# Kernel tuning notes

Measured on AMD Instinct MI355X. Metric: run time of the kernel, lower is better.

Reference implementation:

```python
import jax, jax.numpy as jnp
import numpy as np

N = 50000
F_IN = 128
HID = 64
HEADS = 4
CLASSES = 16
E = 800000
NEG_SLOPE = 0.2


def _gat_layer(x, src, dst, W, a_src, a_dst, bias, heads, ch, concat):
    n = x.shape[0]
    h = (x @ W).reshape(n, heads, ch)                     # [N,H,C]
    alpha_src = jnp.einsum('nhc,hc->nh', h, a_src)        # [N,H]
    alpha_dst = jnp.einsum('nhc,hc->nh', h, a_dst)        # [N,H]
    e = jax.nn.leaky_relu(alpha_src[src] + alpha_dst[dst], NEG_SLOPE)  # [E,H]
    # segment softmax over edges grouped by destination node
    m = jax.ops.segment_max(e, dst, num_segments=n)       # [N,H]
    ex = jnp.exp(e - m[dst])                              # [E,H]
    s = jax.ops.segment_sum(ex, dst, num_segments=n)      # [N,H]
    alpha = ex / (s[dst] + 1e-16)                         # [E,H]
    # weighted scatter-add aggregation of neighbor features
    out = jax.ops.segment_sum(h[src] * alpha[:, :, None], dst, num_segments=n)  # [N,H,C]
    if concat:
        return out.reshape(n, heads * ch) + bias
    return out.mean(axis=1) + bias


def setup_inputs() -> dict:
    key = jax.random.key(0)
    ks = jax.random.split(key, 12)
    x = jax.random.normal(ks[0], (N, F_IN), dtype=jnp.float32)
    edge_index = jax.random.randint(ks[1], (2, E), 0, N, dtype=jnp.int64)
    g1 = 1.0 / np.sqrt(F_IN)
    g2 = 1.0 / np.sqrt(HID * HEADS)
    W1 = jax.random.normal(ks[2], (F_IN, HEADS * HID), dtype=jnp.float32) * g1
    a_src1 = jax.random.normal(ks[3], (HEADS, HID), dtype=jnp.float32) * g1
    a_dst1 = jax.random.normal(ks[4], (HEADS, HID), dtype=jnp.float32) * g1
    b1 = jnp.zeros((HEADS * HID,), dtype=jnp.float32)
    W2 = jax.random.normal(ks[5], (HEADS * HID, CLASSES), dtype=jnp.float32) * g2
    a_src2 = jax.random.normal(ks[6], (1, CLASSES), dtype=jnp.float32) * g2
    a_dst2 = jax.random.normal(ks[7], (1, CLASSES), dtype=jnp.float32) * g2
    b2 = jnp.zeros((CLASSES,), dtype=jnp.float32)
    return {"x": x, "edge_index": edge_index, "W1": W1, "a_src1": a_src1,
            "a_dst1": a_dst1, "b1": b1, "W2": W2, "a_src2": a_src2,
            "a_dst2": a_dst2, "b2": b2}


def reference(x, edge_index, W1, a_src1, a_dst1, b1, W2, a_src2, a_dst2, b2):
    n = x.shape[0]
    # add self-loops (PyG GATConv default add_self_loops=True)
    loops = jnp.arange(n, dtype=edge_index.dtype)
    src = jnp.concatenate([edge_index[0], loops])
    dst = jnp.concatenate([edge_index[1], loops])
    h = _gat_layer(x, src, dst, W1, a_src1, a_dst1, b1, HEADS, HID, concat=True)
    h = jax.nn.elu(h)
    out = _gat_layer(h, src, dst, W2, a_src2, a_dst2, b2, 1, CLASSES, concat=False)
    return jax.nn.log_softmax(out, axis=1)
```

## Files before the change

kernel.cpp:

```cpp
#include <hip/hip_runtime.h>
#include <hip/hip_fp16.h>
#include <math.h>

#define NEG 0.2f

typedef __attribute__((ext_vector_type(8))) short bf16x8;
typedef __attribute__((ext_vector_type(4))) float f32x4;

__device__ __forceinline__ float lrelu(float x){ return x > 0.f ? x : NEG*x; }

__device__ __forceinline__ float bflo(unsigned u){ return __uint_as_float(u << 16); }
__device__ __forceinline__ float bfhi(unsigned u){ return __uint_as_float(u & 0xffff0000u); }

__device__ __forceinline__ float selh(float a0, float a1, float a2, float a3,
                                      bool bit0, bool bit1){
  float lo = bit0 ? a1 : a0;
  float hi = bit0 ? a3 : a2;
  return bit1 ? hi : lo;
}

__device__ __forceinline__ unsigned short f2bf(float x){
  unsigned u = __float_as_uint(x);
  u += 0x7fffu + ((u >> 16) & 1u);
  return (unsigned short)(u >> 16);
}

#define FMA8(e, h) \
  acc[0]=fmaf(e,bflo(h.x),acc[0]); acc[1]=fmaf(e,bfhi(h.x),acc[1]); \
  acc[2]=fmaf(e,bflo(h.y),acc[2]); acc[3]=fmaf(e,bfhi(h.y),acc[3]); \
  acc[4]=fmaf(e,bflo(h.z),acc[4]); acc[5]=fmaf(e,bfhi(h.z),acc[5]); \
  acc[6]=fmaf(e,bflo(h.w),acc[6]); acc[7]=fmaf(e,bfhi(h.w),acc[7]);

__global__ void detect_kernel(const int* __restrict__ ei, int* __restrict__ flag){
  int lane = threadIdx.x;
  int v = ei[2*lane + 1];
  unsigned long long b = __ballot(v != 0);
  if (lane == 0) flag[0] = (b == 0ULL) ? 1 : 0;
}

__global__ void fill_kernel(const int* __restrict__ ei, const int* __restrict__ flag,
                            int* __restrict__ cnt, int* __restrict__ adj, int E){
  int is64 = flag[0];
  int stride = gridDim.x * blockDim.x;
  for (int i = blockIdx.x*blockDim.x + threadIdx.x; i < E; i += stride){
    int s = is64 ? ei[2*i]       : ei[i];
    int d = is64 ? ei[2*(E + i)] : ei[E + i];
    int pos = atomicAdd(&cnt[d], 1);
    if (pos < 64) adj[(d << 6) + pos] = s;
  }
}

__device__ __forceinline__ int wt_addr(int col, int k){
  int g = (k >> 3) ^ (col & 7);
  return col*128 + g*8 + (k & 7);
}

__global__ __launch_bounds__(256) void gemm1_mfma(const float* __restrict__ x,
                             const float* __restrict__ W,
                             const float* __restrict__ asrcw, const float* __restrict__ adstw,
                             unsigned short* __restrict__ h1b,
                             float* __restrict__ as1, float* __restrict__ ad1, int N){
  __shared__ unsigned short wt[256*128];
  int t = threadIdx.x;
  int lane = t & 63, w = t >> 6;
  int row0 = blockIdx.x * 64 + w * 16;

  int arow = row0 + (lane & 15);
  if (arow >= N) arow = N - 1;
  const float* xr = x + (size_t)arow * 128 + (lane >> 4) * 8;
  bf16x8 afrag[4];
  #pragma unroll
  for (int kk = 0; kk < 4; kk++){
    float4 p0 = *reinterpret_cast<const float4*>(xr + kk*32);
    float4 p1 = *reinterpret_cast<const float4*>(xr + kk*32 + 4);
    afrag[kk][0] = (short)f2bf(p0.x); afrag[kk][1] = (short)f2bf(p0.y);
    afrag[kk][2] = (short)f2bf(p0.z); afrag[kk][3] = (short)f2bf(p0.w);
    afrag[kk][4] = (short)f2bf(p1.x); afrag[kk][5] = (short)f2bf(p1.y);
    afrag[kk][6] = (short)f2bf(p1.z); afrag[kk][7] = (short)f2bf(p1.w);
  }

  int c = t;
  for (int k0 = 0; k0 < 128; k0 += 8){
    bf16x8 v;
    #pragma unroll
    for (int j = 0; j < 8; j++) v[j] = (short)f2bf(W[(size_t)(k0+j)*256 + c]);
    *reinterpret_cast<bf16x8*>(&wt[wt_addr(c, k0)]) = v;
  }
  __syncthreads();

  f32x4 acc[16];
  #pragma unroll
  for (int n = 0; n < 16; n++) acc[n] = (f32x4){0.f,0.f,0.f,0.f};
  #pragma unroll
  for (int kk = 0; kk < 4; kk++){
    #pragma unroll
    for (int n = 0; n < 16; n++){
      bf16x8 b = *reinterpret_cast<const bf16x8*>(
          &wt[wt_addr(n*16 + (lane & 15), kk*32 + (lane >> 4)*8)]);
      acc[n] = __builtin_amdgcn_mfma_f32_16x16x32_bf16(afrag[kk], b, acc[n], 0, 0, 0);
    }
  }

  int rbase = row0 + (lane >> 4)*4;
  int cbase = lane & 15;
  #pragma unroll
  for (int n = 0; n < 16; n++){
    #pragma unroll
    for (int r = 0; r < 4; r++){
      int row = rbase + r;
      if (row < N) h1b[(size_t)row*256 + n*16 + cbase] = f2bf(acc[n][r]);
    }
  }

  float av[16], dv[16];
  #pragma unroll
  for (int n = 0; n < 16; n++){
    av[n] = asrcw[n*16 + cbase];
    dv[n] = adstw[n*16 + cbase];
  }
  #pragma unroll
  for (int r = 0; r < 4; r++){
    int row = rbase + r;
    float hs[4], hd[4];
    #pragma unroll
    for (int h = 0; h < 4; h++){
      float ps = 0.f, pd = 0.f;
      #pragma unroll
      for (int q = 0; q < 4; q++){
        int n = h*4 + q;
        ps = fmaf(acc[n][r], av[n], ps);
        pd = fmaf(acc[n][r], dv[n], pd);
      }
      #pragma unroll
      for (int off = 1; off < 16; off <<= 1){
        ps += __shfl_xor(ps, off, 64);
        pd += __shfl_xor(pd, off, 64);
      }
      hs[h] = ps; hd[h] = pd;
    }
    if (cbase == 0 && row < N){
      *reinterpret_cast<float4*>(as1 + (size_t)row*4) = make_float4(hs[0],hs[1],hs[2],hs[3]);
      *reinterpret_cast<float4*>(ad1 + (size_t)row*4) = make_float4(hd[0],hd[1],hd[2],hd[3]);
    }
  }
}

__global__ void edge_exp_kernel(const float* __restrict__ as1, const float* __restrict__ ad1,
                                const int* __restrict__ cnt, const int* __restrict__ adj,
                                __half* __restrict__ exarr, float* __restrict__ den, int N){
  int node = (blockIdx.x*blockDim.x + threadIdx.x) >> 6;
  int lane = threadIdx.x & 63;
  if (node >= N) return;
  int cn = cnt[node]; if (cn > 64) cn = 64;
  int beg = node << 6;
  bool val = lane < cn;
  int src = val ? adj[beg + lane] : 0;
  float4 dv = *reinterpret_cast<const float4*>(ad1 + (size_t)node*4);
  float4 sv = *reinterpret_cast<const float4*>(as1 + (size_t)src*4);
  float ex0 = val ? __expf(lrelu(sv.x + dv.x)) : 0.f;
  float ex1 = val ? __expf(lrelu(sv.y + dv.y)) : 0.f;
  float ex2 = val ? __expf(lrelu(sv.z + dv.z)) : 0.f;
  float ex3 = val ? __expf(lrelu(sv.w + dv.w)) : 0.f;

  if (val){
    __half2 p0 = __floats2half2_rn(ex0, ex1);
    __half2 p1 = __floats2half2_rn(ex2, ex3);
    uint2 o;
    o.x = *reinterpret_cast<unsigned*>(&p0);
    o.y = *reinterpret_cast<unsigned*>(&p1);
    *reinterpret_cast<uint2*>(exarr + (size_t)(beg + lane)*4) = o;
  }

  float sp0 = ex0, sp1 = ex1, sp2 = ex2, sp3 = ex3;
  #pragma unroll
  for (int off = 32; off; off >>= 1){
    sp0 += __shfl_xor(sp0, off, 64);
    sp1 += __shfl_xor(sp1, off, 64);
    sp2 += __shfl_xor(sp2, off, 64);
    sp3 += __shfl_xor(sp3, off, 64);
  }
  float4 s2 = *reinterpret_cast<const float4*>(as1 + (size_t)node*4);
  float exs0 = __expf(lrelu(s2.x + dv.x));
  float exs1 = __expf(lrelu(s2.y + dv.y));
  float exs2 = __expf(lrelu(s2.z + dv.z));
  float exs3 = __expf(lrelu(s2.w + dv.w));
  if (lane == 0){
    *reinterpret_cast<float4*>(den + (size_t)node*8) =
        make_float4(sp0 + exs0, sp1 + exs1, sp2 + exs2, sp3 + exs3);
    *reinterpret_cast<float4*>(den + (size_t)node*8 + 4) =
        make_float4(exs0, exs1, exs2, exs3);
  }
}

__global__ void agg1_kernel(const unsigned short* __restrict__ h1b,
                            const float* __restrict__ b1,
                            const int* __restrict__ cnt, const int* __restrict__ adj,
                            const __half* __restrict__ exarr, const float* __restrict__ den,
                            unsigned short* __restrict__ hact_b, int N){
  int node = (blockIdx.x*blockDim.x + threadIdx.x) >> 6;
  int lane = threadIdx.x & 63;
  if (node >= N) return;
  int cn = cnt[node]; if (cn > 64) cn = 64;
  int beg = node << 6;
  int hf = lane >> 5;
  int sl = lane & 31;
  int hh = sl >> 3;
  bool hb0 = (sl & 8) != 0, hb1 = (sl & 16) != 0;
  const __half* exw = exarr + (size_t)beg*4;
  const int* aj = adj + beg;
  unsigned co = sl*8;

  float acc[8];
  #pragma unroll
  for (int q = 0; q < 8; q++) acc[q] = 0.f;

  int j = 0;
  for (; j + 8 <= cn; j += 8){
    int e0 = j+hf, e1 = j+2+hf, e2 = j+4+hf, e3 = j+6+hf;
    int s0 = aj[e0], s1 = aj[e1], s2 = aj[e2], s3 = aj[e3];
    float w0 = __half2float(exw[e0*4+hh]);
    float w1 = __half2float(exw[e1*4+hh]);
    float w2 = __half2float(exw[e2*4+hh]);
    float w3 = __half2float(exw[e3*4+hh]);
    uint4 h0 = *reinterpret_cast<const uint4*>(h1b + (size_t)s0*256 + co);
    uint4 h1 = *reinterpret_cast<const uint4*>(h1b + (size_t)s1*256 + co);
    uint4 h2 = *reinterpret_cast<const uint4*>(h1b + (size_t)s2*256 + co);
    uint4 h3 = *reinterpret_cast<const uint4*>(h1b + (size_t)s3*256 + co);
    FMA8(w0, h0); FMA8(w1, h1); FMA8(w2, h2); FMA8(w3, h3);
  }
  for (; j + 4 <= cn; j += 4){
    int e0 = j+hf, e1 = j+2+hf;
    int s0 = aj[e0], s1 = aj[e1];
    float w0 = __half2float(exw[e0*4+hh]);
    float w1 = __half2float(exw[e1*4+hh]);
    uint4 h0 = *reinterpret_cast<const uint4*>(h1b + (size_t)s0*256 + co);
    uint4 h1 = *reinterpret_cast<const uint4*>(h1b + (size_t)s1*256 + co);
    FMA8(w0, h0); FMA8(w1, h1);
  }
  for (; j < cn; j += 2){
    if (j + hf < cn){
      int e0 = j+hf;
      int s0 = aj[e0];
      float w0 = __half2float(exw[e0*4+hh]);
      uint4 h0 = *reinterpret_cast<const uint4*>(h1b + (size_t)s0*256 + co);
      FMA8(w0, h0);
    }
  }

  #pragma unroll
  for (int q = 0; q < 8; q++) acc[q] += __shfl_xor(acc[q], 32, 64);

  if (hf == 0){
    float4 dn  = *reinterpret_cast<const float4*>(den + (size_t)node*8);
    float4 dsf = *reinterpret_cast<const float4*>(den + (size_t)node*8 + 4);
    float dh  = selh(dn.x, dn.y, dn.z, dn.w, hb0, hb1);
    float ehs = selh(dsf.x, dsf.y, dsf.z, dsf.w, hb0, hb1);
    uint4 hv = *reinterpret_cast<const uint4*>(h1b + (size_t)node*256 + co);
    FMA8(ehs, hv);

    float rinv = 1.0f / (dh + 1e-16f);
    float4 bA = *reinterpret_cast<const float4*>(b1 + sl*8);
    float4 bB = *reinterpret_cast<const float4*>(b1 + sl*8 + 4);
    float o[8];
    o[0] = acc[0]*rinv + bA.x; o[1] = acc[1]*rinv + bA.y;
    o[2] = acc[2]*rinv + bA.z; o[3] = acc[3]*rinv + bA.w;
    o[4] = acc[4]*rinv + bB.x; o[5] = acc[5]*rinv + bB.y;
    o[6] = acc[6]*rinv + bB.z; o[7] = acc[7]*rinv + bB.w;
    #pragma unroll
    for (int q = 0; q < 8; q++) o[q] = o[q] > 0.f ? o[q] : expm1f(o[q]);
    uint4 ob;
    ob.x = (unsigned)f2bf(o[0]) | ((unsigned)f2bf(o[1]) << 16);
    ob.y = (unsigned)f2bf(o[2]) | ((unsigned)f2bf(o[3]) << 16);
    ob.z = (unsigned)f2bf(o[4]) | ((unsigned)f2bf(o[5]) << 16);
    ob.w = (unsigned)f2bf(o[6]) | ((unsigned)f2bf(o[7]) << 16);
    *reinterpret_cast<uint4*>(hact_b + (size_t)node*256 + co) = ob;
  }
}

__device__ __forceinline__ int wt2_addr(int col, int k){
  int g = (k >> 3) ^ (col & 7);
  return col*256 + g*8 + (k & 7);
}

__global__ __launch_bounds__(256) void gemm2_mfma(const unsigned short* __restrict__ hact_b,
                             const float* __restrict__ W2,
                             const float* __restrict__ asrc2, const float* __restrict__ adst2,
                             float* __restrict__ h2, float* __restrict__ as2,
                             float* __restrict__ ad2, int N){
  __shared__ unsigned short wt[16*256];
  int t = threadIdx.x;
  int lane = t & 63, w = t >> 6;
  int row0 = blockIdx.x * 64 + w * 16;

  {
    float4 r0 = *reinterpret_cast<const float4*>(W2 + (size_t)t*16);
    float4 r1 = *reinterpret_cast<const float4*>(W2 + (size_t)t*16 + 4);
    float4 r2 = *reinterpret_cast<const float4*>(W2 + (size_t)t*16 + 8);
    float4 r3 = *reinterpret_cast<const float4*>(W2 + (size_t)t*16 + 12);
    float wr[16] = {r0.x,r0.y,r0.z,r0.w, r1.x,r1.y,r1.z,r1.w,
                    r2.x,r2.y,r2.z,r2.w, r3.x,r3.y,r3.z,r3.w};
    #pragma unroll
    for (int cc = 0; cc < 16; cc++) wt[wt2_addr(cc, t)] = f2bf(wr[cc]);
  }

  int arow = row0 + (lane & 15);
  if (arow >= N) arow = N - 1;
  const unsigned short* hr = hact_b + (size_t)arow*256 + (lane >> 4)*8;
  __syncthreads();

  f32x4 acc = (f32x4){0.f,0.f,0.f,0.f};
  #pragma unroll
  for (int kk = 0; kk < 8; kk++){
    bf16x8 a = *reinterpret_cast<const bf16x8*>(hr + kk*32);
    bf16x8 b = *reinterpret_cast<const bf16x8*>(
        &wt[wt2_addr(lane & 15, kk*32 + (lane >> 4)*8)]);
    acc = __builtin_amdgcn_mfma_f32_16x16x32_bf16(a, b, acc, 0, 0, 0);
  }

  int rbase = row0 + (lane >> 4)*4;
  int cbase = lane & 15;
  float avc = asrc2[cbase], dvc = adst2[cbase];
  #pragma unroll
  for (int r = 0; r < 4; r++){
    int row = rbase + r;
    if (row < N) h2[(size_t)row*16 + cbase] = acc[r];
    float ps = acc[r]*avc, pd = acc[r]*dvc;
    #pragma unroll
    for (int off = 1; off < 16; off <<= 1){
      ps += __shfl_xor(ps, off, 64);
      pd += __shfl_xor(pd, off, 64);
    }
    if (cbase == 0 && row < N){ as2[row] = ps; ad2[row] = pd; }
  }
}

__global__ void agg2_kernel(const float* __restrict__ h2, const float* __restrict__ as2,
                            const float* __restrict__ ad2, const float* __restrict__ b2,
                            const int* __restrict__ cnt, const int* __restrict__ adj,
                            float* __restrict__ out, int N){
  __shared__ float exlds[4][64];
  __shared__ int   srclds[4][64];
  int node = (blockIdx.x*blockDim.x + threadIdx.x) >> 6;
  int lane = threadIdx.x & 63;
  int w = (threadIdx.x >> 6) & 3;
  if (node >= N) return;
  int cn = cnt[node]; if (cn > 64) cn = 64;
  int beg_ = node << 6;
  float adn = ad2[node];
  int g = lane >> 4, c = lane & 15;
  float sp = 0.f, acc = 0.f;

  {
    bool val = lane < cn;
    int srcl = val ? adj[beg_ + lane] : 0;
    float e = val ? lrelu(as2[srcl] + adn) : -3e38f;
    float ex = __expf(e);
    sp += ex;
    exlds[w][lane] = ex;
    srclds[w][lane] = srcl;

    #pragma unroll 2
    for (int j = g; j < cn; j += 4){
      int src = srclds[w][j];
      float eh = exlds[w][j];
      acc = fmaf(eh, h2[(size_t)src*16 + c], acc);
    }
  }

  #pragma unroll
  for (int off = 32; off; off >>= 1) sp += __shfl_xor(sp, off, 64);
  acc += __shfl_xor(acc, 16, 64);
  acc += __shfl_xor(acc, 32, 64);

  float eself = __expf(lrelu(as2[node] + adn));
  sp += eself;
  if (g == 0){
    acc = fmaf(eself, h2[(size_t)node*16 + c], acc);
    float v = acc / (sp + 1e-16f) + b2[c];
    float mx = v;
    #pragma unroll
    for (int off = 1; off < 16; off <<= 1) mx = fmaxf(mx, __shfl_xor(mx, off, 64));
    float se = __expf(v - mx);
    #pragma unroll
    for (int off = 1; off < 16; off <<= 1) se += __shfl_xor(se, off, 64);
    out[(size_t)node*16 + c] = v - mx - logf(se);
  }
}

extern "C" void kernel_launch(void* const* d_in, const int* in_sizes, int n_in,
                              void* d_out, int out_size, void* d_ws, size_t ws_size,
                              hipStream_t stream){
  const float* x    = (const float*)d_in[0];
  const int*   ei   = (const int*)d_in[1];
  const float* W1   = (const float*)d_in[2];
  const float* as1w = (const float*)d_in[3];
  const float* ad1w = (const float*)d_in[4];
  const float* b1   = (const float*)d_in[5];
  const float* W2   = (const float*)d_in[6];
  const float* as2w = (const float*)d_in[7];
  const float* ad2w = (const float*)d_in[8];
  const float* b2   = (const float*)d_in[9];
  float* out = (float*)d_out;

  int N = in_sizes[0] / 128;
  int E = in_sizes[1] / 2;

  char* p = (char*)d_ws;
  size_t off = 0;
  auto alloc = [&](size_t b){ size_t c = off; off = (off + b + 255) & ~(size_t)255; return c; };
  unsigned short* h1b   = (unsigned short*)(p + alloc((size_t)N*256*2));
  unsigned short* hact_b= (unsigned short*)(p + alloc((size_t)N*256*2));
  float* h2     = (float*)(p + alloc((size_t)N*16*4));
  float* as1    = (float*)(p + alloc((size_t)N*4*4));
  float* ad1    = (float*)(p + alloc((size_t)N*4*4));
  float* as2    = (float*)(p + alloc((size_t)N*4));
  float* ad2    = (float*)(p + alloc((size_t)N*4));
  int*   cnt    = (int*)(p + alloc((size_t)N*4));
  int*   adj    = (int*)(p + alloc((size_t)N*64*4));
  __half* exarr = (__half*)(p + alloc((size_t)N*64*4*2));
  float* den    = (float*)(p + alloc((size_t)N*8*4));
  int*   flag   = (int*)(p + alloc(4));

  hipMemsetAsync(cnt, 0, (size_t)N*4, stream);
  detect_kernel<<<1, 64, 0, stream>>>(ei, flag);
  fill_kernel<<<2048, 256, 0, stream>>>(ei, flag, cnt, adj, E);

  gemm1_mfma<<<(N + 63)/64, 256, 0, stream>>>(x, W1, as1w, ad1w, h1b, as1, ad1, N);
  edge_exp_kernel<<<(N*64 + 255)/256, 256, 0, stream>>>(as1, ad1, cnt, adj, exarr, den, N);
  agg1_kernel<<<(N*64 + 255)/256, 256, 0, stream>>>(h1b, b1, cnt, adj, exarr, den, hact_b, N);
  gemm2_mfma<<<(N + 63)/64, 256, 0, stream>>>(hact_b, W2, as2w, ad2w, h2, as2, ad2, N);
  agg2_kernel<<<(N*64 + 255)/256, 256, 0, stream>>>(h2, as2, ad2, b2, cnt, adj, out, N);
}
```

Measured before the change: 190.9 us.

## Split layer-2 aggregation into separate edge-exp and aggregate kernels

```diff
diff --git a/kernel.cpp b/kernel.cpp
--- a/kernel.cpp
+++ b/kernel.cpp
@@ -334,49 +334,60 @@
   }
 }
 
-__global__ void agg2_kernel(const float* __restrict__ h2, const float* __restrict__ as2,
-                            const float* __restrict__ ad2, const float* __restrict__ b2,
-                            const int* __restrict__ cnt, const int* __restrict__ adj,
-                            float* __restrict__ out, int N){
-  __shared__ float exlds[4][64];
-  __shared__ int   srclds[4][64];
+__global__ void edge_exp2_kernel(const float* __restrict__ as2, const float* __restrict__ ad2,
+                                 const int* __restrict__ cnt, const int* __restrict__ adj,
+                                 float* __restrict__ wex, float2* __restrict__ den2, int N){
   int node = (blockIdx.x*blockDim.x + threadIdx.x) >> 6;
   int lane = threadIdx.x & 63;
-  int w = (threadIdx.x >> 6) & 3;
   if (node >= N) return;
   int cn = cnt[node]; if (cn > 64) cn = 64;
-  int beg_ = node << 6;
+  int beg = node << 6;
   float adn = ad2[node];
+  bool val = lane < cn;
+  int src = val ? adj[beg + lane] : 0;
+  float wv = val ? __expf(lrelu(as2[src] + adn)) : 0.f;
+  if (val) wex[beg + lane] = wv;
+  float sp = wv;
+  #pragma unroll
+  for (int off = 32; off; off >>= 1) sp += __shfl_xor(sp, off, 64);
+  float eself = __expf(lrelu(as2[node] + adn));
+  if (lane == 0) den2[node] = make_float2(sp + eself, eself);
+}
+
+__global__ void agg2_kernel(const float* __restrict__ h2, const float* __restrict__ b2,
+                            const int* __restrict__ cnt, const int* __restrict__ adj,
+                            const float* __restrict__ wex, const float2* __restrict__ den2,
+                            float* __restrict__ out, int N){
+  int node = (blockIdx.x*blockDim.x + threadIdx.x) >> 6;
+  int lane = threadIdx.x & 63;
+  if (node >= N) return;
+  int cn = cnt[node]; if (cn > 64) cn = 64;
+  int beg = node << 6;
   int g = lane >> 4, c = lane & 15;
-  float sp = 0.f, acc = 0.f;
-
-  {
-    bool val = lane < cn;
-    int srcl = val ? adj[beg_ + lane] : 0;
-    float e = val ? lrelu(as2[srcl] + adn) : -3e38f;
-    float ex = __expf(e);
-    sp += ex;
-    exlds[w][lane] = ex;
-    srclds[w][lane] = srcl;
-
-    #pragma unroll 2
-    for (int j = g; j < cn; j += 4){
-      int src = srclds[w][j];
-      float eh = exlds[w][j];
-      acc = fmaf(eh, h2[(size_t)src*16 + c], acc);
-    }
-  }
-
-  #pragma unroll
-  for (int off = 32; off; off >>= 1) sp += __shfl_xor(sp, off, 64);
+  float acc = 0.f;
+
+  int j = g;
+  for (; j + 4 < cn; j += 8){
+    int   s0 = adj[beg + j],  s1 = adj[beg + j + 4];
+    float w0 = wex[beg + j],  w1 = wex[beg + j + 4];
+    float v0 = h2[(size_t)s0*16 + c];
+    float v1 = h2[(size_t)s1*16 + c];
+    acc = fmaf(w0, v0, acc);
+    acc = fmaf(w1, v1, acc);
+  }
+  if (j < cn){
+    int   s0 = adj[beg + j];
+    float w0 = wex[beg + j];
+    acc = fmaf(w0, h2[(size_t)s0*16 + c], acc);
+  }
+
   acc += __shfl_xor(acc, 16, 64);
   acc += __shfl_xor(acc, 32, 64);
 
-  float eself = __expf(lrelu(as2[node] + adn));
-  sp += eself;
   if (g == 0){
-    acc = fmaf(eself, h2[(size_t)node*16 + c], acc);
-    float v = acc / (sp + 1e-16f) + b2[c];
+    float2 dn = den2[node];
+    acc = fmaf(dn.y, h2[(size_t)node*16 + c], acc);
+    float v = acc / (dn.x + 1e-16f) + b2[c];
     float mx = v;
     #pragma unroll
     for (int off = 1; off < 16; off <<= 1) mx = fmaxf(mx, __shfl_xor(mx, off, 64));
@@ -419,6 +430,8 @@
   int*   adj    = (int*)(p + alloc((size_t)N*64*4));
   __half* exarr = (__half*)(p + alloc((size_t)N*64*4*2));
   float* den    = (float*)(p + alloc((size_t)N*8*4));
+  float* wex    = (float*)(p + alloc((size_t)N*64*4));
+  float2* den2  = (float2*)(p + alloc((size_t)N*8));
   int*   flag   = (int*)(p + alloc(4));
 
   hipMemsetAsync(cnt, 0, (size_t)N*4, stream);
@@ -429,5 +442,6 @@
   edge_exp_kernel<<<(N*64 + 255)/256, 256, 0, stream>>>(as1, ad1, cnt, adj, exarr, den, N);
   agg1_kernel<<<(N*64 + 255)/256, 256, 0, stream>>>(h1b, b1, cnt, adj, exarr, den, hact_b, N);
   gemm2_mfma<<<(N + 63)/64, 256, 0, stream>>>(hact_b, W2, as2w, ad2w, h2, as2, ad2, N);
-  agg2_kernel<<<(N*64 + 255)/256, 256, 0, stream>>>(h2, as2, ad2, b2, cnt, adj, out, N);
-}
+  edge_exp2_kernel<<<(N*64 + 255)/256, 256, 0, stream>>>(as2, ad2, cnt, adj, wex, den2, N);
+  agg2_kernel<<<(N*64 + 255)/256, 256, 0, stream>>>(h2, b2, cnt, adj, wex, den2, out, N);
+}
```

Measured after the change: 203.3 us. 6.5% more time.
